# Performance work log

Hardware: AMD Instinct MI355X
Metric: run time of the kernel (lower is better)

## Reference

```python
import jax, jax.numpy as jnp
import numpy as np

B, D, A, R = 256, 1024, 1024, 8  # batch, feat_dim, ada_dim, rank
I = A  # inter_dim defaults to ada_dim
LN_EPS = 1e-5


def setup_inputs() -> dict:
    key = jax.random.key(0)
    ks = jax.random.split(key, 5)
    return {
        "x": jax.random.normal(ks[0], (B, D), jnp.float32),
        "ada_emb": jax.random.normal(ks[1], (B, A), jnp.float32),
        "base_layer": jax.random.normal(ks[2], (D, D), jnp.float32) * 0.02,
        "ln_gamma": jnp.ones((A,), jnp.float32),
        "ln_beta": jnp.zeros((A,), jnp.float32),
        "W1": jax.random.normal(ks[3], (A, I), jnp.float32) * 0.02,
        "b1": jnp.zeros((I,), jnp.float32),
        "W2": jax.random.normal(ks[4], (I, D * R * 2), jnp.float32) * 0.02,
        "b2": jnp.zeros((D * R * 2,), jnp.float32),
    }


def reference(x, ada_emb, base_layer, ln_gamma, ln_beta, W1, b1, W2, b2):
    Bc, Dc = x.shape
    # norm_cond: LayerNorm over ada_dim
    mu = jnp.mean(ada_emb, axis=-1, keepdims=True)
    var = jnp.var(ada_emb, axis=-1, keepdims=True)
    cond = (ada_emb - mu) * jax.lax.rsqrt(var + LN_EPS) * ln_gamma + ln_beta
    # gen_weight: Linear -> GELU (exact, erf) -> Linear
    h = jax.nn.gelu(cond @ W1 + b1, approximate=False)
    w = h @ W2 + b2                      # [B, 2*D*R]
    x_a, x_b = jnp.split(w, 2, axis=-1)
    x_a = x_a.reshape(Bc, Dc, R)         # [B, D, R]
    x_b = x_b.reshape(Bc, Dc, R)         # [B, D, R]
    # per-sample low-rank weight added to the shared base layer
    layer = base_layer[None, :, :] + jnp.einsum('bdr,bkr->bdk', x_a, x_b)  # [B, D, D]
    out = jnp.einsum('bc,bco->bo', x, layer)
    return x + out  # residual=True
```

## Files before the change

kernel.cpp:

```cpp
#include <hip/hip_runtime.h>
#include <math.h>

#define BB 256
#define DD 1024
#define AA 1024
#define RR 8
#define II 1024
#define NOUT (2*DD*RR)
#define LN_EPS 1e-5f

typedef __attribute__((ext_vector_type(8))) short bf16x8;
typedef __attribute__((ext_vector_type(4))) float f32x4;

typedef const __attribute__((address_space(1))) unsigned int gu32_t;
typedef __attribute__((address_space(3))) unsigned int lu32_t;

__device__ __forceinline__ void glds16(void* lds, const void* g) {
    __builtin_amdgcn_global_load_lds((gu32_t*)g, (lu32_t*)lds, 16, 0, 0);
}

__device__ __forceinline__ f32x4 mfma16(bf16x8 a, bf16x8 b, f32x4 c) {
    return __builtin_amdgcn_mfma_f32_16x16x32_bf16(a, b, c, 0, 0, 0);
}

__device__ __forceinline__ unsigned short f2bf(float x) {
    unsigned int u = __float_as_uint(x);
    unsigned int r = (u + 0x7fffu + ((u >> 16) & 1u)) >> 16;
    return (unsigned short)r;
}
__device__ __forceinline__ float bf2f(unsigned short b) {
    return __uint_as_float(((unsigned int)b) << 16);
}
__device__ __forceinline__ void split2(float x, unsigned short& hi, unsigned short& lo) {
    hi = f2bf(x);
    lo = f2bf(x - bf2f(hi));
}

__device__ __forceinline__ float gelu_exact(float v) {
    return 0.5f * v * (1.0f + erff(v * 0.70710678118654752f));
}

__global__ __launch_bounds__(256) void ln_split_kernel(const float* __restrict__ ada,
                                                       const float* __restrict__ xp,
                                                       const float* __restrict__ gamma,
                                                       const float* __restrict__ beta,
                                                       unsigned short* __restrict__ c_hi,
                                                       unsigned short* __restrict__ c_lo,
                                                       unsigned short* __restrict__ x_hi,
                                                       unsigned short* __restrict__ x_lo) {
    const int b = blockIdx.x;
    const int tid = threadIdx.x;
    const float4 v = ((const float4*)(ada + (size_t)b * AA))[tid];

    float s  = v.x + v.y + v.z + v.w;
    float ss = v.x * v.x + v.y * v.y + v.z * v.z + v.w * v.w;
    #pragma unroll
    for (int off = 32; off; off >>= 1) {
        s  += __shfl_down(s, off);
        ss += __shfl_down(ss, off);
    }
    __shared__ float red[2][4];
    const int wid = tid >> 6, lane = tid & 63;
    if (lane == 0) { red[0][wid] = s; red[1][wid] = ss; }
    __syncthreads();
    __shared__ float stats[2];
    if (tid == 0) {
        float S  = red[0][0] + red[0][1] + red[0][2] + red[0][3];
        float SS = red[1][0] + red[1][1] + red[1][2] + red[1][3];
        float mu  = S * (1.0f / AA);
        float var = SS * (1.0f / AA) - mu * mu;
        stats[0] = mu;
        stats[1] = rsqrtf(var + LN_EPS);
    }
    __syncthreads();
    const float mu = stats[0], inv = stats[1];
    const float4 g  = ((const float4*)gamma)[tid];
    const float4 be = ((const float4*)beta)[tid];
    float o[4];
    o[0] = (v.x - mu) * inv * g.x + be.x;
    o[1] = (v.y - mu) * inv * g.y + be.y;
    o[2] = (v.z - mu) * inv * g.z + be.z;
    o[3] = (v.w - mu) * inv * g.w + be.w;
    ushort4 H, L;
    split2(o[0], H.x, L.x); split2(o[1], H.y, L.y);
    split2(o[2], H.z, L.z); split2(o[3], H.w, L.w);
    ((ushort4*)(c_hi + (size_t)b * AA))[tid] = H;
    ((ushort4*)(c_lo + (size_t)b * AA))[tid] = L;

    const float4 xv = ((const float4*)(xp + (size_t)b * DD))[tid];
    split2(xv.x, H.x, L.x); split2(xv.y, H.y, L.y);
    split2(xv.z, H.z, L.z); split2(xv.w, H.w, L.w);
    ((ushort4*)(x_hi + (size_t)b * DD))[tid] = H;
    ((ushort4*)(x_lo + (size_t)b * DD))[tid] = L;
}

__global__ __launch_bounds__(256) void gemm_small(const unsigned short* __restrict__ x_hi,
                                                  const unsigned short* __restrict__ x_lo,
                                                  const unsigned short* __restrict__ c_hi,
                                                  const unsigned short* __restrict__ c_lo,
                                                  const float* __restrict__ base,
                                                  const float* __restrict__ W1,
                                                  const float* __restrict__ b1,
                                                  float* __restrict__ outy,
                                                  unsigned short* __restrict__ h_hi,
                                                  unsigned short* __restrict__ h_lo) {
    __shared__ __align__(16) unsigned short As[2][4096];
    __shared__ __align__(16) unsigned short Bs[2][8192];

    const int z = blockIdx.z;
    const unsigned short* __restrict__ Ahi = z ? c_hi : x_hi;
    const unsigned short* __restrict__ Alo = z ? c_lo : x_lo;
    const float* __restrict__ Bsrc = z ? W1 : base;

    const int tid = threadIdx.x;
    const int bn = blockIdx.x * 64;
    const int bm = blockIdx.y * 32;
    const int wid = tid >> 6, l = tid & 63;
    const int wn = wid;
    const int kg = l >> 4;
    const int lr16 = (l & 15) * 16;

    f32x4 acc[2];
    acc[0] = (f32x4)0.0f; acc[1] = (f32x4)0.0f;

    const int sn = tid & 63;
    const int s_nb = sn >> 4, s_lane16 = (sn & 15) * 16;
    const int s_k4 = (tid >> 6) * 4;

    float v[4][4];

    #define SB_LOAD(K0)                                                         \
        _Pragma("unroll")                                                       \
        for (int p = 0; p < 4; p++) {                                           \
            const int kq = s_k4 + p * 16;                                       \
            _Pragma("unroll")                                                   \
            for (int i = 0; i < 4; i++)                                         \
                v[p][i] = Bsrc[(size_t)((K0) + kq + i) * 1024 + bn + sn];       \
        }

    #define SB_WRITE(BUF)                                                       \
        _Pragma("unroll")                                                       \
        for (int p = 0; p < 4; p++) {                                           \
            const int kq = s_k4 + p * 16;                                       \
            const int kidx = kq >> 3, klow2 = (kq & 7) * 2;                     \
            ushort4 H, L;                                                       \
            split2(v[p][0], H.x, L.x); split2(v[p][1], H.y, L.y);               \
            split2(v[p][2], H.z, L.z); split2(v[p][3], H.w, L.w);               \
            *(ushort4*)((char*)Bs[BUF] + ((0*4 + s_nb)*8 + kidx)*256 + s_lane16 + klow2) = H; \
            *(ushort4*)((char*)Bs[BUF] + ((1*4 + s_nb)*8 + kidx)*256 + s_lane16 + klow2) = L; \
        }

    #define SA_GLDS(BUF, K0)                                                    \
        _Pragma("unroll")                                                       \
        for (int c = 0; c < 2; c++) {                                           \
            const int ch = wid * 2 + c;                               \
            const int pl = ch >> 2, rr = ch & 3;                                \
            const int m = rr & 1, half = rr >> 1;                               \
            const unsigned short* src = (pl ? Alo : Ahi)                        \
                + (size_t)(bm + m * 16 + (l & 15)) * 1024 + (K0) + half * 32 + kg * 8; \
            glds16((char*)As[BUF] + ((pl*2 + m)*8 + half*4) * 256, src);        \
        }

    #define S_COMPUTE(BUF)                                                      \
        {                                                                       \
            _Pragma("unroll")                                                   \
            for (int s = 0; s < 2; s++) {                                       \
                bf16x8 a[2][2], bbf[2];                                         \
                _Pragma("unroll")                                               \
                for (int pl = 0; pl < 2; pl++) {                                \
                    _Pragma("unroll")                                           \
                    for (int mi = 0; mi < 2; mi++)                              \
                        a[pl][mi] = *(const bf16x8*)((const char*)As[BUF] +     \
                            ((pl*2 + mi)*8 + s*4 + kg)*256 + lr16);             \
                    bbf[pl] = *(const bf16x8*)((const char*)Bs[BUF] +           \
                            ((pl*4 + wn)*8 + s*4 + kg)*256 + lr16);             \
                }                                                               \
                _Pragma("unroll")                                               \
                for (int mi = 0; mi < 2; mi++) {                                \
                    acc[mi] = mfma16(a[0][mi], bbf[0], acc[mi]);                \
                    acc[mi] = mfma16(a[0][mi], bbf[1], acc[mi]);                \
                    acc[mi] = mfma16(a[1][mi], bbf[0], acc[mi]);                \
                }                                                               \
            }                                                                   \
        }

    SB_LOAD(0);
    SA_GLDS(0, 0);
    SB_WRITE(0);
    __syncthreads();

    int cur = 0;
    for (int t = 0; t < 16; ++t) {
        if (t < 15) {
            const int k0n = (t + 1) * 64;
            SB_LOAD(k0n);
            SA_GLDS(cur ^ 1, k0n);
        }
        S_COMPUTE(cur);
        if (t < 15) {
            SB_WRITE(cur ^ 1);
            __syncthreads();
        }
        cur ^= 1;
    }

    #pragma unroll
    for (int mi = 0; mi < 2; mi++) {
        const int row0 = bm + mi * 16 + (l >> 4) * 4;
        const int col  = bn + wn * 16 + (l & 15);
        #pragma unroll
        for (int j = 0; j < 4; j++) {
            float val = acc[mi][j];
            if (z == 0) {
                outy[(size_t)(row0 + j) * 1024 + col] = val;
            } else {
                float g = gelu_exact(val + b1[col]);
                unsigned short hi, lo;
                split2(g, hi, lo);
                h_hi[(size_t)(row0 + j) * 1024 + col] = hi;
                h_lo[(size_t)(row0 + j) * 1024 + col] = lo;
            }
        }
    }
    #undef SB_LOAD
    #undef SB_WRITE
    #undef SA_GLDS
    #undef S_COMPUTE
}

__global__ __launch_bounds__(256) void gemm_big(const unsigned short* __restrict__ Ahi,
                                                const unsigned short* __restrict__ Alo,
                                                const float* __restrict__ Bm,
                                                const float* __restrict__ bias,
                                                float* __restrict__ Cm) {
    __shared__ __align__(16) unsigned short As[2][8192];
    __shared__ __align__(16) unsigned short Bs[2][8192];

    const int tid = threadIdx.x;
    const int bn = blockIdx.x * 128;
    const int bm = blockIdx.y * 128;
    const int wid = tid >> 6, l = tid & 63;
    const int wm = wid >> 1, wn = wid & 1;
    const int kg = l >> 4;
    const int lr16 = (l & 15) * 16;

    f32x4 acc[4][4];
    #pragma unroll
    for (int i = 0; i < 4; i++)
        #pragma unroll
        for (int j = 0; j < 4; j++) acc[i][j] = (f32x4)0.0f;

    const int sn = tid & 127;
    const int s_nb = sn >> 4, s_lane16 = (sn & 15) * 16;
    const int s_kb = (tid >> 7) * 4;

    float v[4][4];

    #define GB_LOAD(K0)                                                         \
        _Pragma("unroll")                                                       \
        for (int p = 0; p < 4; p++) {                                           \
            const int kq = s_kb + p * 8;                                        \
            _Pragma("unroll")                                                   \
            for (int i = 0; i < 4; i++)                                         \
                v[p][i] = Bm[(size_t)((K0) + kq + i) * NOUT + bn + sn];         \
        }

    #define GB_WRITE(BUF)                                                       \
        _Pragma("unroll")                                                       \
        for (int p = 0; p < 4; p++) {                                           \
            ushort4 H, L;                                                       \
            split2(v[p][0], H.x, L.x); split2(v[p][1], H.y, L.y);               \
            split2(v[p][2], H.z, L.z); split2(v[p][3], H.w, L.w);               \
            *(ushort4*)((char*)Bs[BUF] + ((0*8 + s_nb)*4 + p)*256 + s_lane16 + s_kb*2) = H; \
            *(ushort4*)((char*)Bs[BUF] + ((1*8 + s_nb)*4 + p)*256 + s_lane16 + s_kb*2) = L; \
        }

    #define GA_GLDS(BUF, K0)                                                    \
        _Pragma("unroll")                                                       \
        for (int c = 0; c < 4; c++) {                                           \
            const int ch = wid * 4 + c;                              \
            const int pl = ch >> 3, m = ch & 7;                                 \
            const unsigned short* src = (pl ? Alo : Ahi)                        \
                + (size_t)(bm + m * 16 + (l & 15)) * II + (K0) + kg * 8;        \
            glds16((char*)As[BUF] + ch * 1024, src);                            \
        }

    #define G_COMPUTE(BUF)                                                     \
        {                                                                       \
            bf16x8 a[2][4], bbf[2][4];                                          \
            _Pragma("unroll")                                                   \
            for (int pl = 0; pl < 2; pl++) {                                    \
                _Pragma("unroll")                                               \
                for (int mi = 0; mi < 4; mi++)                                  \
                    a[pl][mi] = *(const bf16x8*)((const char*)As[BUF] +         \
                        ((pl*8 + wm*4 + mi)*4 + kg)*256 + lr16);                \
                _Pragma("unroll")                                               \
                for (int ni = 0; ni < 4; ni++)                                  \
                    bbf[pl][ni] = *(const bf16x8*)((const char*)Bs[BUF] +       \
                        ((pl*8 + wn*4 + ni)*4 + kg)*256 + lr16);                \
            }                                                                   \
            _Pragma("unroll")                                                   \
            for (int mi = 0; mi < 4; mi++) {                                    \
                _Pragma("unroll")                                               \
                for (int ni = 0; ni < 4; ni++) {                                \
                    acc[mi][ni] = mfma16(a[0][mi], bbf[0][ni], acc[mi][ni]);    \
                    acc[mi][ni] = mfma16(a[0][mi], bbf[1][ni], acc[mi][ni]);    \
                    acc[mi][ni] = mfma16(a[1][mi], bbf[0][ni], acc[mi][ni]);    \
                }                                                               \
            }                                                                   \
        }

    GB_LOAD(0);
    GA_GLDS(0, 0);
    GB_WRITE(0);
    __syncthreads();

    int cur = 0;
    for (int t = 0; t < 32; ++t) {
        if (t < 31) {
            const int k0n = (t + 1) * 32;
            GB_LOAD(k0n);
            GA_GLDS(cur ^ 1, k0n);
        }
        G_COMPUTE(cur);
        if (t < 31) {
            GB_WRITE(cur ^ 1);
            __syncthreads();
        }
        cur ^= 1;
    }

    #pragma unroll
    for (int mi = 0; mi < 4; mi++) {
        #pragma unroll
        for (int ni = 0; ni < 4; ni++) {
            const int row0 = bm + wm * 64 + mi * 16 + (l >> 4) * 4;
            const int col  = bn + wn * 64 + ni * 16 + (l & 15);
            const float bv = bias[col];
            #pragma unroll
            for (int j = 0; j < 4; j++)
                Cm[(size_t)(row0 + j) * NOUT + col] = acc[mi][ni][j] + bv;
        }
    }
    #undef GB_LOAD
    #undef GB_WRITE
    #undef GA_GLDS
    #undef G_COMPUTE
}

__global__ __launch_bounds__(256) void tail_kernel(const float* __restrict__ x,
                                                   const float* __restrict__ w,
                                                   float* __restrict__ out) {
    const int b = blockIdx.x;
    const int tid = threadIdx.x;
    const float* wa = w + (size_t)b * NOUT;
    const float4 xv = ((const float4*)(x + (size_t)b * DD))[tid];
    const float xs[4] = {xv.x, xv.y, xv.z, xv.w};

    float acc[RR] = {};
    #pragma unroll
    for (int i = 0; i < 4; i++) {
        const int c = tid * 4 + i;
        const float4 w0 = *(const float4*)&wa[c * RR];
        const float4 w1 = *(const float4*)&wa[c * RR + 4];
        acc[0] = fmaf(xs[i], w0.x, acc[0]);
        acc[1] = fmaf(xs[i], w0.y, acc[1]);
        acc[2] = fmaf(xs[i], w0.z, acc[2]);
        acc[3] = fmaf(xs[i], w0.w, acc[3]);
        acc[4] = fmaf(xs[i], w1.x, acc[4]);
        acc[5] = fmaf(xs[i], w1.y, acc[5]);
        acc[6] = fmaf(xs[i], w1.z, acc[6]);
        acc[7] = fmaf(xs[i], w1.w, acc[7]);
    }
    __shared__ float red[4][RR];
    __shared__ float trs[RR];
    const int wid = tid >> 6, lane = tid & 63;
    #pragma unroll
    for (int r = 0; r < RR; r++) {
        float vv = acc[r];
        #pragma unroll
        for (int off = 32; off; off >>= 1) vv += __shfl_down(vv, off);
        if (lane == 0) red[wid][r] = vv;
    }
    __syncthreads();
    if (tid < RR) trs[tid] = red[0][tid] + red[1][tid] + red[2][tid] + red[3][tid];
    __syncthreads();

    float tr[RR];
    #pragma unroll
    for (int r = 0; r < RR; r++) tr[r] = trs[r];

    const float* wb = wa + DD * RR;
    const int o0 = tid * 4;
    const float4 yv = *(const float4*)&out[(size_t)b * DD + o0];

    float vals[4];
    #pragma unroll
    for (int i = 0; i < 4; i++) {
        const float4 w0 = *(const float4*)&wb[(o0 + i) * RR];
        const float4 w1 = *(const float4*)&wb[(o0 + i) * RR + 4];
        vals[i] = tr[0] * w0.x + tr[1] * w0.y + tr[2] * w0.z + tr[3] * w0.w
                + tr[4] * w1.x + tr[5] * w1.y + tr[6] * w1.z + tr[7] * w1.w;
    }
    float4 o;
    o.x = xv.x + yv.x + vals[0];
    o.y = xv.y + yv.y + vals[1];
    o.z = xv.z + yv.z + vals[2];
    o.w = xv.w + yv.w + vals[3];
    *(float4*)&out[(size_t)b * DD + o0] = o;
}

extern "C" void kernel_launch(void* const* d_in, const int* in_sizes, int n_in,
                              void* d_out, int out_size, void* d_ws, size_t ws_size,
                              hipStream_t stream) {
    const float* x     = (const float*)d_in[0];
    const float* ada   = (const float*)d_in[1];
    const float* base  = (const float*)d_in[2];
    const float* gamma = (const float*)d_in[3];
    const float* beta  = (const float*)d_in[4];
    const float* W1    = (const float*)d_in[5];
    const float* b1    = (const float*)d_in[6];
    const float* W2    = (const float*)d_in[7];
    const float* b2    = (const float*)d_in[8];
    float* out = (float*)d_out;

    char* wsb = (char*)d_ws;
    float* w = (float*)(wsb);
    unsigned short* h_hi = (unsigned short*)(wsb + 16777216);
    unsigned short* h_lo = (unsigned short*)(wsb + 17301504);
    unsigned short* x_hi = (unsigned short*)(wsb + 17825792);
    unsigned short* x_lo = (unsigned short*)(wsb + 18350080);
    unsigned short* c_hi = (unsigned short*)(wsb + 18874368);
    unsigned short* c_lo = (unsigned short*)(wsb + 19398656);

    ln_split_kernel<<<BB, 256, 0, stream>>>(ada, x, gamma, beta, c_hi, c_lo, x_hi, x_lo);

    gemm_small<<<dim3(1024 / 64, BB / 32, 2), 256, 0, stream>>>(
        x_hi, x_lo, c_hi, c_lo, base, W1, b1, out, h_hi, h_lo);

    gemm_big<<<dim3(NOUT / 128, BB / 128), 256, 0, stream>>>(h_hi, h_lo, W2, b2, w);

    tail_kernel<<<BB, 256, 0, stream>>>(x, w, out);
}
```

Measured before the change: 202.3 us.

## Retile big GEMM to 128x64 with XCD-aware swizzle, vectorize B-stage writes, add setprio

The large W2 GEMM tile shrinks from 128x128 to 128x64, giving 512 blocks instead of 256, with a 1D grid swizzled so neighbouring blocks share A rows. Both GEMMs now have each thread load 8 consecutive k values and write the split bf16 hi/lo pairs to LDS as one 16-byte vector store instead of several 8-byte stores. s_setprio is raised around the MFMA bursts, and the loop-end barrier is made unconditional. The aim is better occupancy and load balance across CUs and fewer LDS store instructions. The cost is that the A tile is re-read from global memory twice as often across the grid.

```diff
diff --git a/kernel.cpp b/kernel.cpp
--- a/kernel.cpp
+++ b/kernel.cpp
@@ -10,6 +10,7 @@
 #define LN_EPS 1e-5f
 
 typedef __attribute__((ext_vector_type(8))) short bf16x8;
+typedef __attribute__((ext_vector_type(8))) unsigned short ushort8;
 typedef __attribute__((ext_vector_type(4))) float f32x4;
 
 typedef const __attribute__((address_space(1))) unsigned int gu32_t;
@@ -116,72 +117,71 @@
     const int bn = blockIdx.x * 64;
     const int bm = blockIdx.y * 32;
     const int wid = tid >> 6, l = tid & 63;
-    const int wn = wid;
-    const int kg = l >> 4;
-    const int lr16 = (l & 15) * 16;
+    const int kg = l >> 4, lr16 = (l & 15) * 16;
 
     f32x4 acc[2];
     acc[0] = (f32x4)0.0f; acc[1] = (f32x4)0.0f;
 
     const int sn = tid & 63;
-    const int s_nb = sn >> 4, s_lane16 = (sn & 15) * 16;
-    const int s_k4 = (tid >> 6) * 4;
-
-    float v[4][4];
-
-    #define SB_LOAD(K0)                                                         \
-        _Pragma("unroll")                                                       \
-        for (int p = 0; p < 4; p++) {                                           \
-            const int kq = s_k4 + p * 16;                                       \
-            _Pragma("unroll")                                                   \
-            for (int i = 0; i < 4; i++)                                         \
-                v[p][i] = Bsrc[(size_t)((K0) + kq + i) * 1024 + bn + sn];       \
-        }
-
-    #define SB_WRITE(BUF)                                                       \
-        _Pragma("unroll")                                                       \
-        for (int p = 0; p < 4; p++) {                                           \
-            const int kq = s_k4 + p * 16;                                       \
-            const int kidx = kq >> 3, klow2 = (kq & 7) * 2;                     \
-            ushort4 H, L;                                                       \
-            split2(v[p][0], H.x, L.x); split2(v[p][1], H.y, L.y);               \
-            split2(v[p][2], H.z, L.z); split2(v[p][3], H.w, L.w);               \
-            *(ushort4*)((char*)Bs[BUF] + ((0*4 + s_nb)*8 + kidx)*256 + s_lane16 + klow2) = H; \
-            *(ushort4*)((char*)Bs[BUF] + ((1*4 + s_nb)*8 + kidx)*256 + s_lane16 + klow2) = L; \
-        }
-
-    #define SA_GLDS(BUF, K0)                                                    \
-        _Pragma("unroll")                                                       \
-        for (int c = 0; c < 2; c++) {                                           \
-            const int ch = wid * 2 + c;                               \
-            const int pl = ch >> 2, rr = ch & 3;                                \
-            const int m = rr & 1, half = rr >> 1;                               \
-            const unsigned short* src = (pl ? Alo : Ahi)                        \
-                + (size_t)(bm + m * 16 + (l & 15)) * 1024 + (K0) + half * 32 + kg * 8; \
-            glds16((char*)As[BUF] + ((pl*2 + m)*8 + half*4) * 256, src);        \
-        }
-
-    #define S_COMPUTE(BUF)                                                      \
-        {                                                                       \
-            _Pragma("unroll")                                                   \
-            for (int s = 0; s < 2; s++) {                                       \
-                bf16x8 a[2][2], bbf[2];                                         \
-                _Pragma("unroll")                                               \
-                for (int pl = 0; pl < 2; pl++) {                                \
-                    _Pragma("unroll")                                           \
-                    for (int mi = 0; mi < 2; mi++)                              \
-                        a[pl][mi] = *(const bf16x8*)((const char*)As[BUF] +     \
-                            ((pl*2 + mi)*8 + s*4 + kg)*256 + lr16);             \
-                    bbf[pl] = *(const bf16x8*)((const char*)Bs[BUF] +           \
-                            ((pl*4 + wn)*8 + s*4 + kg)*256 + lr16);             \
-                }                                                               \
-                _Pragma("unroll")                                               \
-                for (int mi = 0; mi < 2; mi++) {                                \
-                    acc[mi] = mfma16(a[0][mi], bbf[0], acc[mi]);                \
-                    acc[mi] = mfma16(a[0][mi], bbf[1], acc[mi]);                \
-                    acc[mi] = mfma16(a[1][mi], bbf[0], acc[mi]);                \
-                }                                                               \
-            }                                                                   \
+    const int s_nb = sn >> 4, s_l16 = (sn & 15) * 16;
+
+    float v[2][8];
+
+    #define SB_LOAD(K0)                                                          \
+        _Pragma("unroll")                                                        \
+        for (int h = 0; h < 2; h++) {                                            \
+            const int c2 = (tid >> 6) * 2 + h;              \
+            _Pragma("unroll")                                                    \
+            for (int j = 0; j < 8; j++)                                          \
+                v[h][j] = Bsrc[(size_t)((K0) + c2 * 8 + j) * 1024 + bn + sn];    \
+        }
+
+    #define SB_WRITE(BUF)                                                        \
+        _Pragma("unroll")                                                        \
+        for (int h = 0; h < 2; h++) {                                            \
+            const int c2 = (tid >> 6) * 2 + h;                                   \
+            ushort8 H, L;                                                        \
+            _Pragma("unroll")                                                    \
+            for (int j = 0; j < 8; j++) { unsigned short hh, ll;                 \
+                split2(v[h][j], hh, ll); H[j] = hh; L[j] = ll; }                 \
+            *(ushort8*)((char*)Bs[BUF] + ((0*4 + s_nb)*8 + c2)*256 + s_l16) = H; \
+            *(ushort8*)((char*)Bs[BUF] + ((1*4 + s_nb)*8 + c2)*256 + s_l16) = L; \
+        }
+
+    #define SA_GLDS(BUF, K0)                                                     \
+        _Pragma("unroll")                                                        \
+        for (int c = 0; c < 2; c++) {                                            \
+            const int ch = wid * 2 + c;                                \
+            const int pl = ch >> 2, sub = ch & 3;                                \
+            const int mb = sub >> 1, half = sub & 1;                             \
+            const unsigned short* src = (pl ? Alo : Ahi)                         \
+                + (size_t)(bm + mb * 16 + (l & 15)) * 1024 + (K0) + half * 32 + kg * 8; \
+            glds16((char*)As[BUF] + (pl*2 + mb)*2048 + half*1024, src);          \
+        }
+
+    #define S_COMPUTE(BUF)                                                       \
+        {                                                                        \
+            _Pragma("unroll")                                                    \
+            for (int s = 0; s < 2; s++) {                                        \
+                bf16x8 a[2][2], bbf[2];                                          \
+                _Pragma("unroll")                                                \
+                for (int pl = 0; pl < 2; pl++) {                                 \
+                    _Pragma("unroll")                                            \
+                    for (int mi = 0; mi < 2; mi++)                               \
+                        a[pl][mi] = *(const bf16x8*)((const char*)As[BUF] +      \
+                            ((pl*2 + mi)*8 + s*4 + kg)*256 + lr16);              \
+                    bbf[pl] = *(const bf16x8*)((const char*)Bs[BUF] +            \
+                            ((pl*4 + wid)*8 + s*4 + kg)*256 + lr16);             \
+                }                                                                \
+                __builtin_amdgcn_s_setprio(1);                                   \
+                _Pragma("unroll")                                                \
+                for (int mi = 0; mi < 2; mi++) {                                 \
+                    acc[mi] = mfma16(a[0][mi], bbf[0], acc[mi]);                 \
+                    acc[mi] = mfma16(a[0][mi], bbf[1], acc[mi]);                 \
+                    acc[mi] = mfma16(a[1][mi], bbf[0], acc[mi]);                 \
+                }                                                                \
+                __builtin_amdgcn_s_setprio(0);                                   \
+            }                                                                    \
         }
 
     SB_LOAD(0);
@@ -199,15 +199,15 @@
         S_COMPUTE(cur);
         if (t < 15) {
             SB_WRITE(cur ^ 1);
-            __syncthreads();
-        }
+        }
+        __syncthreads();
         cur ^= 1;
     }
 
     #pragma unroll
     for (int mi = 0; mi < 2; mi++) {
-        const int row0 = bm + mi * 16 + (l >> 4) * 4;
-        const int col  = bn + wn * 16 + (l & 15);
+        const int row0 = bm + mi * 16 + kg * 4;
+        const int col  = bn + wid * 16 + (l & 15);
         #pragma unroll
         for (int j = 0; j < 4; j++) {
             float val = acc[mi][j];
@@ -234,80 +234,78 @@
                                                 const float* __restrict__ bias,
                                                 float* __restrict__ Cm) {
     __shared__ __align__(16) unsigned short As[2][8192];
-    __shared__ __align__(16) unsigned short Bs[2][8192];
+    __shared__ __align__(16) unsigned short Bs[2][4096];
+
+    const int orig = blockIdx.x;
+    const int swz  = ((orig & 7) << 6) + (orig >> 3);
+    const int bn = (swz >> 1) * 64;
+    const int bm = (swz & 1) * 128;
 
     const int tid = threadIdx.x;
-    const int bn = blockIdx.x * 128;
-    const int bm = blockIdx.y * 128;
     const int wid = tid >> 6, l = tid & 63;
     const int wm = wid >> 1, wn = wid & 1;
-    const int kg = l >> 4;
-    const int lr16 = (l & 15) * 16;
-
-    f32x4 acc[4][4];
-    #pragma unroll
-    for (int i = 0; i < 4; i++)
-        #pragma unroll
-        for (int j = 0; j < 4; j++) acc[i][j] = (f32x4)0.0f;
-
-    const int sn = tid & 127;
-    const int s_nb = sn >> 4, s_lane16 = (sn & 15) * 16;
-    const int s_kb = (tid >> 7) * 4;
-
-    float v[4][4];
-
-    #define GB_LOAD(K0)                                                         \
-        _Pragma("unroll")                                                       \
-        for (int p = 0; p < 4; p++) {                                           \
-            const int kq = s_kb + p * 8;                                        \
-            _Pragma("unroll")                                                   \
-            for (int i = 0; i < 4; i++)                                         \
-                v[p][i] = Bm[(size_t)((K0) + kq + i) * NOUT + bn + sn];         \
-        }
-
-    #define GB_WRITE(BUF)                                                       \
-        _Pragma("unroll")                                                       \
-        for (int p = 0; p < 4; p++) {                                           \
-            ushort4 H, L;                                                       \
-            split2(v[p][0], H.x, L.x); split2(v[p][1], H.y, L.y);               \
-            split2(v[p][2], H.z, L.z); split2(v[p][3], H.w, L.w);               \
-            *(ushort4*)((char*)Bs[BUF] + ((0*8 + s_nb)*4 + p)*256 + s_lane16 + s_kb*2) = H; \
-            *(ushort4*)((char*)Bs[BUF] + ((1*8 + s_nb)*4 + p)*256 + s_lane16 + s_kb*2) = L; \
-        }
-
-    #define GA_GLDS(BUF, K0)                                                    \
-        _Pragma("unroll")                                                       \
-        for (int c = 0; c < 4; c++) {                                           \
-            const int ch = wid * 4 + c;                              \
-            const int pl = ch >> 3, m = ch & 7;                                 \
-            const unsigned short* src = (pl ? Alo : Ahi)                        \
-                + (size_t)(bm + m * 16 + (l & 15)) * II + (K0) + kg * 8;        \
-            glds16((char*)As[BUF] + ch * 1024, src);                            \
-        }
-
-    #define G_COMPUTE(BUF)                                                     \
-        {                                                                       \
-            bf16x8 a[2][4], bbf[2][4];                                          \
-            _Pragma("unroll")                                                   \
-            for (int pl = 0; pl < 2; pl++) {                                    \
-                _Pragma("unroll")                                               \
-                for (int mi = 0; mi < 4; mi++)                                  \
-                    a[pl][mi] = *(const bf16x8*)((const char*)As[BUF] +         \
-                        ((pl*8 + wm*4 + mi)*4 + kg)*256 + lr16);                \
-                _Pragma("unroll")                                               \
-                for (int ni = 0; ni < 4; ni++)                                  \
-                    bbf[pl][ni] = *(const bf16x8*)((const char*)Bs[BUF] +       \
-                        ((pl*8 + wn*4 + ni)*4 + kg)*256 + lr16);                \
-            }                                                                   \
-            _Pragma("unroll")                                                   \
-            for (int mi = 0; mi < 4; mi++) {                                    \
-                _Pragma("unroll")                                               \
-                for (int ni = 0; ni < 4; ni++) {                                \
-                    acc[mi][ni] = mfma16(a[0][mi], bbf[0][ni], acc[mi][ni]);    \
-                    acc[mi][ni] = mfma16(a[0][mi], bbf[1][ni], acc[mi][ni]);    \
-                    acc[mi][ni] = mfma16(a[1][mi], bbf[0][ni], acc[mi][ni]);    \
-                }                                                               \
-            }                                                                   \
+    const int kg = l >> 4, lr16 = (l & 15) * 16;
+
+    f32x4 acc[4][2];
+    #pragma unroll
+    for (int i = 0; i < 4; i++) { acc[i][0] = (f32x4)0.0f; acc[i][1] = (f32x4)0.0f; }
+
+    const int sn = tid & 63;
+    const int skc = tid >> 6;
+    const int s_nb = sn >> 4, s_l16 = (sn & 15) * 16;
+
+    float v[8];
+
+    #define GB_LOAD(K0)                                                          \
+        _Pragma("unroll")                                                        \
+        for (int j = 0; j < 8; j++)                                              \
+            v[j] = Bm[(size_t)((K0) + skc * 8 + j) * NOUT + bn + sn];
+
+    #define GB_WRITE(BUF)                                                        \
+        {                                                                        \
+            ushort8 H, L;                                                        \
+            _Pragma("unroll")                                                    \
+            for (int j = 0; j < 8; j++) { unsigned short hh, ll;                 \
+                split2(v[j], hh, ll); H[j] = hh; L[j] = ll; }                    \
+            *(ushort8*)((char*)Bs[BUF] + ((0*4 + s_nb)*4 + skc)*256 + s_l16) = H;\
+            *(ushort8*)((char*)Bs[BUF] + ((1*4 + s_nb)*4 + skc)*256 + s_l16) = L;\
+        }
+
+    #define GA_GLDS(BUF, K0)                                                     \
+        _Pragma("unroll")                                                        \
+        for (int c = 0; c < 4; c++) {                                            \
+            const int ch = wid * 4 + c;                               \
+            const int pl = ch >> 3, mb = ch & 7;                                 \
+            const unsigned short* src = (pl ? Alo : Ahi)                         \
+                + (size_t)(bm + mb * 16 + (l & 15)) * II + (K0) + kg * 8;        \
+            glds16((char*)As[BUF] + ch * 1024, src);                             \
+        }
+
+    #define G_COMPUTE(BUF)                                                       \
+        {                                                                        \
+            bf16x8 a[2][4], bbf[2][2];                                           \
+            _Pragma("unroll")                                                    \
+            for (int pl = 0; pl < 2; pl++) {                                     \
+                _Pragma("unroll")                                                \
+                for (int mi = 0; mi < 4; mi++)                                   \
+                    a[pl][mi] = *(const bf16x8*)((const char*)As[BUF] +          \
+                        ((pl*8 + wm*4 + mi)*4 + kg)*256 + lr16);                 \
+                _Pragma("unroll")                                                \
+                for (int ni = 0; ni < 2; ni++)                                   \
+                    bbf[pl][ni] = *(const bf16x8*)((const char*)Bs[BUF] +        \
+                        ((pl*4 + wn*2 + ni)*4 + kg)*256 + lr16);                 \
+            }                                                                    \
+            __builtin_amdgcn_s_setprio(1);                                       \
+            _Pragma("unroll")                                                    \
+            for (int mi = 0; mi < 4; mi++) {                                     \
+                _Pragma("unroll")                                                \
+                for (int ni = 0; ni < 2; ni++) {                                 \
+                    acc[mi][ni] = mfma16(a[0][mi], bbf[0][ni], acc[mi][ni]);     \
+                    acc[mi][ni] = mfma16(a[0][mi], bbf[1][ni], acc[mi][ni]);     \
+                    acc[mi][ni] = mfma16(a[1][mi], bbf[0][ni], acc[mi][ni]);     \
+                }                                                                \
+            }                                                                    \
+            __builtin_amdgcn_s_setprio(0);                                       \
         }
 
     GB_LOAD(0);
@@ -325,17 +323,17 @@
         G_COMPUTE(cur);
         if (t < 31) {
             GB_WRITE(cur ^ 1);
-            __syncthreads();
-        }
+        }
+        __syncthreads();
         cur ^= 1;
     }
 
     #pragma unroll
     for (int mi = 0; mi < 4; mi++) {
         #pragma unroll
-        for (int ni = 0; ni < 4; ni++) {
-            const int row0 = bm + wm * 64 + mi * 16 + (l >> 4) * 4;
-            const int col  = bn + wn * 64 + ni * 16 + (l & 15);
+        for (int ni = 0; ni < 2; ni++) {
+            const int row0 = bm + wm * 64 + mi * 16 + kg * 4;
+            const int col  = bn + wn * 32 + ni * 16 + (l & 15);
             const float bv = bias[col];
             #pragma unroll
             for (int j = 0; j < 4; j++)
@@ -438,7 +436,7 @@
     gemm_small<<<dim3(1024 / 64, BB / 32, 2), 256, 0, stream>>>(
         x_hi, x_lo, c_hi, c_lo, base, W1, b1, out, h_hi, h_lo);
 
-    gemm_big<<<dim3(NOUT / 128, BB / 128), 256, 0, stream>>>(h_hi, h_lo, W2, b2, w);
+    gemm_big<<<512, 256, 0, stream>>>(h_hi, h_lo, W2, b2, w);
 
     tail_kernel<<<BB, 256, 0, stream>>>(x, w, out);
 }
```

Measured after the change: 186.5 us. 1.08x faster.
